# Optimization experiments

Measured on AMD Instinct MI355X. Metric: run time of the kernel, lower is better.

## Reference

```python
import jax, jax.numpy as jnp
import numpy as np

B, C, H, W = 256, 256, 16, 16   # batch, backbone channels, spatial (H*W = 256 = loop count)
E, NCLS = 128, 200              # opt.embed_size, opt.class_num

def _conv(x, w, stride, pad):
    # NCHW / OIHW conv, explicit torch-style symmetric padding
    return jax.lax.conv_general_dilated(x, w, (stride, stride), [(pad, pad), (pad, pad)],
                                        dimension_numbers=('NCHW', 'OIHW', 'NCHW'))

def _bn(x, s, b):
    # eval-mode BatchNorm folded to per-channel scale + shift
    return x * s[None, :, None, None] + b[None, :, None, None]

def setup_inputs() -> dict:
    key = jax.random.key(0)
    ks = jax.random.split(key, 12)
    f = lambda k, shape, scale: jax.random.normal(k, shape, jnp.float32) * scale
    bn_s = lambda k, n: 1.0 + 0.05 * jax.random.normal(k, (n,), jnp.float32)
    bn_b = lambda k, n: 0.05 * jax.random.normal(k, (n,), jnp.float32)
    return {
        'x': f(ks[0], (B, C, H, W), 1.0),
        'embed_w': f(ks[1], (E, C), 0.05),
        'embed_b': f(ks[2], (E,), 0.05),
        'b1_conv1': f(ks[3], (512, 256, 3, 3), 0.03),
        'b1_bn1_s': bn_s(jax.random.fold_in(key, 101), 512),
        'b1_bn1_b': bn_b(jax.random.fold_in(key, 102), 512),
        'b1_conv2': f(ks[4], (512, 512, 3, 3), 0.02),
        'b1_bn2_s': bn_s(jax.random.fold_in(key, 103), 512),
        'b1_bn2_b': bn_b(jax.random.fold_in(key, 104), 512),
        'b1_down_w': f(ks[5], (512, 256, 1, 1), 0.05),
        'b1_down_s': bn_s(jax.random.fold_in(key, 105), 512),
        'b1_down_b': bn_b(jax.random.fold_in(key, 106), 512),
        'b2_conv1': f(ks[6], (512, 512, 3, 3), 0.02),
        'b2_bn1_s': bn_s(jax.random.fold_in(key, 107), 512),
        'b2_bn1_b': bn_b(jax.random.fold_in(key, 108), 512),
        'b2_conv2': f(ks[7], (512, 512, 3, 3), 0.02),
        'b2_bn2_s': bn_s(jax.random.fold_in(key, 109), 512),
        'b2_bn2_b': bn_b(jax.random.fold_in(key, 110), 512),
        'head_w': f(ks[8], (NCLS, 512), 0.05),
    }

def reference(x, embed_w, embed_b,
              b1_conv1, b1_bn1_s, b1_bn1_b, b1_conv2, b1_bn2_s, b1_bn2_b,
              b1_down_w, b1_down_s, b1_down_b,
              b2_conv1, b2_bn1_s, b2_bn1_b, b2_conv2, b2_bn2_s, b2_bn2_b,
              head_w):
    # --- resblock = resnet layer4 (two BasicBlocks, 256->512, stride 2) ---
    y = jax.nn.relu(_bn(_conv(x, b1_conv1, 2, 1), b1_bn1_s, b1_bn1_b))
    y = _bn(_conv(y, b1_conv2, 1, 1), b1_bn2_s, b1_bn2_b)
    sc = _bn(_conv(x, b1_down_w, 2, 0), b1_down_s, b1_down_b)
    y = jax.nn.relu(y + sc)                              # [B,512,8,8]
    z = jax.nn.relu(_bn(_conv(y, b2_conv1, 1, 1), b2_bn1_s, b2_bn1_b))
    z = _bn(_conv(z, b2_conv2, 1, 1), b2_bn2_s, b2_bn2_b)
    z = jax.nn.relu(z + y)
    # --- class prediction: global avg pool + bias-free linear ---
    feat = jnp.mean(z, axis=(2, 3))                      # [B,512]
    prediction = feat @ head_w.T                         # [B,NCLS]
    # --- consistency: 1x1-conv embedding, then pairwise Gram + sigmoid ---
    emb = jnp.einsum('bchw,ec->behw', x, embed_w) + embed_b[None, :, None, None]
    emb = emb.reshape(B, E, H * W)                       # [B,E,256]
    inv_sqrt_e = jnp.float32(1.0 / np.sqrt(E))
    # vol[b,q,i] = sum_c emb[b,c,i]*emb[b,c,q] / sqrt(E)  (matches the 256-iter loop)
    vol = jax.nn.sigmoid(jnp.einsum('bei,beq->bqi', emb, emb) * inv_sqrt_e)
    return (prediction, vol)
```

## Files before the change

### kernel.cpp

```cpp
#include <hip/hip_runtime.h>


using short8 = __attribute__((ext_vector_type(8))) short;
using f32x4  = __attribute__((ext_vector_type(4))) float;
typedef unsigned short u16;
typedef unsigned int   u32;

#define MFMA(a,b,c) __builtin_amdgcn_mfma_f32_16x16x32_bf16((a),(b),(c),0,0,0)

__device__ __forceinline__ u16 f2b(float f){
    u32 u = __builtin_bit_cast(u32, f);
    u += 0x7FFFu + ((u >> 16) & 1u);
    return (u16)(u >> 16);
}
__device__ __forceinline__ float b2f(u16 h){
    u32 u = ((u32)h) << 16;
    return __builtin_bit_cast(float, u);
}
__device__ __forceinline__ u32 pack2(float a, float b){
    return (u32)f2b(a) | ((u32)f2b(b) << 16);
}
__device__ __forceinline__ float sigmoidf_(float v){
    return 1.0f / (1.0f + __expf(-v));
}

__global__ __launch_bounds__(256)
void prep_kernel(const float* __restrict__ w1, const float* __restrict__ s1,
                 const float* __restrict__ w2, const float* __restrict__ s2,
                 const float* __restrict__ w3, const float* __restrict__ s3,
                 const float* __restrict__ w4, const float* __restrict__ s4,
                 const float* __restrict__ wd, const float* __restrict__ sd,
                 const float* __restrict__ ew,
                 u16* __restrict__ wp1, u16* __restrict__ wp2,
                 u16* __restrict__ wp3, u16* __restrict__ wp4,
                 u16* __restrict__ wpd, u16* __restrict__ wpe)
{
    const int N2 = 9*16*512*40, N1 = 9*8*512*40, ND = 8*512*40, NE = 8*128*40;
    int t = blockIdx.x * 256 + threadIdx.x;
    if (t < N2) {
        int j = t % 40; int r = t / 40; int co = r & 511; int q = r >> 9;
        int cc = q & 15; int dydx = q >> 4;
        float v = (j < 32) ? w2[(co*512 + cc*32 + j)*9 + dydx] * s2[co] : 0.f;
        wp2[t] = f2b(v); return;
    }
    t -= N2;
    if (t < N2) {
        int j = t % 40; int r = t / 40; int co = r & 511; int q = r >> 9;
        int cc = q & 15; int dydx = q >> 4;
        float v = (j < 32) ? w3[(co*512 + cc*32 + j)*9 + dydx] * s3[co] : 0.f;
        wp3[t] = f2b(v); return;
    }
    t -= N2;
    if (t < N2) {
        int j = t % 40; int r = t / 40; int co = r & 511; int q = r >> 9;
        int cc = q & 15; int dydx = q >> 4;
        float v = (j < 32) ? w4[(co*512 + cc*32 + j)*9 + dydx] * s4[co] : 0.f;
        wp4[t] = f2b(v); return;
    }
    t -= N2;
    if (t < N1) {
        int j = t % 40; int r = t / 40; int co = r & 511; int q = r >> 9;
        int cc = q & 7; int dydx = q >> 3;
        float v = (j < 32) ? w1[(co*256 + cc*32 + j)*9 + dydx] * s1[co] : 0.f;
        wp1[t] = f2b(v); return;
    }
    t -= N1;
    if (t < ND) {
        int j = t % 40; int r = t / 40; int co = r & 511; int cc = r >> 9;
        float v = (j < 32) ? wd[co*256 + cc*32 + j] * sd[co] : 0.f;
        wpd[t] = f2b(v); return;
    }
    t -= ND;
    if (t < NE) {
        int j = t % 40; int r = t / 40; int e = r & 127; int cc = r >> 7;
        float v = (j < 32) ? ew[e*256 + cc*32 + j] : 0.f;
        wpe[t] = f2b(v);
    }
}

__global__ __launch_bounds__(512, 2)
void conv1_kernel(const float* __restrict__ x, const u16* __restrict__ wp,
                  const float* __restrict__ bnb, u16* __restrict__ out)
{
    const int cot = blockIdx.x;
    const int b0  = blockIdx.y * 2;
    const int tid = threadIdx.x;
    const int wid = tid >> 6, lane = tid & 63;
    const int ln = lane & 15, kg = lane >> 4;
    const int wco = wid >> 1;
    const int bb  = wid & 1;

    __shared__ u16 actb[2][2*289*40];

    {
        short8 zz = {0,0,0,0,0,0,0,0};
        short8* ab = (short8*)&actb[0][0];
        for (int j = tid; j < 2*2*289*40/8; j += 512) ab[j] = zz;
    }
    __syncthreads();

    auto stage_act = [&](int cc, int p){
        #pragma unroll
        for (int it = 0; it < 16; ++it){
            int f = it*512 + tid;
            int bb2 = f >> 12; int rem = f & 4095;
            int cip = rem >> 8; int px = rem & 255;
            const float* src = &x[(((size_t)(b0+bb2)*256 + cc*32 + 2*cip)*256) + px];
            float v0 = src[0], v1 = src[256];
            int r = ((px >> 4) + 1)*17 + (px & 15) + 1;
            *(u32*)&actb[p][(bb2*289 + r)*40 + 2*cip] = pack2(v0, v1);
        }
    };

    stage_act(0, 0);
    __syncthreads();

    f32x4 zero4 = {0.f,0.f,0.f,0.f};
    f32x4 acc[4][4];
    #pragma unroll
    for (int mf = 0; mf < 4; ++mf)
        #pragma unroll
        for (int nf = 0; nf < 4; ++nf) acc[mf][nf] = zero4;

    int bbase[4];
    #pragma unroll
    for (int nf = 0; nf < 4; ++nf){
        int px = nf*16 + ln;
        bbase[nf] = (bb*289 + 34*(px>>3) + 2*(px&7))*40 + kg*8;
    }

    for (int cc = 0; cc < 8; ++cc){
        if (cc < 7) stage_act(cc+1, (cc+1) & 1);
        const u16* abp = actb[cc & 1];
        #pragma unroll
        for (int d = 0; d < 9; ++d){
            const u16* wdp = wp + ((size_t)(d*8 + cc)*512 + cot*256)*40;
            int dy = d/3, dx = d - dy*3;
            int shift = (dy*17 + dx)*40;
            short8 A[4];
            #pragma unroll
            for (int mf = 0; mf < 4; ++mf)
                A[mf] = *(const short8*)&wdp[(wco*64 + mf*16 + ln)*40 + kg*8];
            #pragma unroll
            for (int nf = 0; nf < 4; ++nf){
                short8 B = *(const short8*)&abp[bbase[nf] + shift];
                #pragma unroll
                for (int mf = 0; mf < 4; ++mf)
                    acc[mf][nf] = MFMA(A[mf], B, acc[mf][nf]);
            }
        }
        __syncthreads();
    }

    #pragma unroll
    for (int mf = 0; mf < 4; ++mf){
        int co0 = cot*256 + wco*64 + mf*16 + kg*4;
        float4 bv = *(const float4*)&bnb[co0];
        #pragma unroll
        for (int nf = 0; nf < 4; ++nf){
            int px = nf*16 + ln;
            size_t o = (((size_t)(b0+bb)*64) + px)*512 + co0;
            f32x4 a = acc[mf][nf];
            ushort4 st;
            st.x = f2b(fmaxf(a[0] + bv.x, 0.f));
            st.y = f2b(fmaxf(a[1] + bv.y, 0.f));
            st.z = f2b(fmaxf(a[2] + bv.z, 0.f));
            st.w = f2b(fmaxf(a[3] + bv.w, 0.f));
            *(ushort4*)&out[o] = st;
        }
    }
}

template<int DOWN, int RES>
__global__ __launch_bounds__(64, 2)
void conv_s1_kernel(const u16* __restrict__ in, const u16* __restrict__ wp,
                    const float* __restrict__ bnb,
                    const float* __restrict__ x, const u16* __restrict__ wpd,
                    const float* __restrict__ dbb,
                    const u16* __restrict__ res, u16* __restrict__ out)
{
    const int b   = blockIdx.x;
    const int cot = blockIdx.y;
    const int lane = threadIdx.x;
    const int ln = lane & 15, kg = lane >> 4;

    __shared__ u16 actb[2][100*40];

    {
        short8 zz = {0,0,0,0,0,0,0,0};
        short8* ab = (short8*)&actb[0][0];
        #pragma unroll
        for (int it = 0; it < 16; ++it){
            int j = it*64 + lane;
            if (j < 1000) ab[j] = zz;
        }
    }

    int s_ld[4]; size_t s_go[4];
    #pragma unroll
    for (int it = 0; it < 4; ++it){
        int j = it*64 + lane;
        int px = j >> 2, cg = j & 3;
        s_ld[it] = (((px>>3)+1)*10 + (px&7) + 1)*40 + cg*8;
        s_go[it] = (((size_t)b*64 + px)*512) + cg*8;
    }

    short8 sreg[4];
    auto stage_load = [&](int cc){
        #pragma unroll
        for (int it = 0; it < 4; ++it)
            sreg[it] = *(const short8*)&in[s_go[it] + cc*32];
    };
    auto stage_store = [&](int p){
        #pragma unroll
        for (int it = 0; it < 4; ++it)
            *(short8*)&actb[p][s_ld[it]] = sreg[it];
    };

    stage_load(0); stage_store(0);

    f32x4 zero4 = {0.f,0.f,0.f,0.f};
    f32x4 acc[4][4];
    #pragma unroll
    for (int mf = 0; mf < 4; ++mf)
        #pragma unroll
        for (int nf = 0; nf < 4; ++nf) acc[mf][nf] = zero4;

    int bro[4];
    #pragma unroll
    for (int nf = 0; nf < 4; ++nf){
        int px = nf*16 + ln;
        bro[nf] = ((px>>3)*10 + (px&7))*40 + kg*8;
    }
    const int aoff = ln*40 + kg*8;
    const int abase = cot*64*40;

    for (int cc = 0; cc < 16; ++cc){
        if (cc < 15) stage_load(cc+1);
        const u16* abp = actb[cc & 1];
        #pragma unroll
        for (int dy = 0; dy < 3; ++dy){
            short8 A[3][4];
            #pragma unroll
            for (int dx = 0; dx < 3; ++dx){
                const u16* wdp = wp + (size_t)((dy*3+dx)*16 + cc)*512*40 + abase;
                #pragma unroll
                for (int mf = 0; mf < 4; ++mf)
                    A[dx][mf] = *(const short8*)&wdp[mf*640 + aoff];
            }
            #pragma unroll
            for (int dx = 0; dx < 3; ++dx){
                int shift = (dy*10 + dx)*40;
                #pragma unroll
                for (int nf = 0; nf < 4; ++nf){
                    short8 B = *(const short8*)&abp[bro[nf] + shift];
                    #pragma unroll
                    for (int mf = 0; mf < 4; ++mf)
                        acc[mf][nf] = MFMA(A[dx][mf], B, acc[mf][nf]);
                }
            }
        }
        if (cc < 15) stage_store((cc+1) & 1);
    }

    if (DOWN){
        for (int dc = 0; dc < 8; ++dc){
            #pragma unroll
            for (int it = 0; it < 16; ++it){
                int f = it*64 + lane;
                int cip = f >> 6, px2 = f & 63;
                int ipx = (px2>>3)*32 + (px2&7)*2;
                const float* src = &x[(((size_t)b*256 + dc*32 + 2*cip)*256) + ipx];
                *(u32*)&actb[0][px2*40 + cip*2] = pack2(src[0], src[256]);
            }
            const u16* wdp = wpd + (size_t)(dc*512)*40 + abase;
            short8 A[4];
            #pragma unroll
            for (int mf = 0; mf < 4; ++mf)
                A[mf] = *(const short8*)&wdp[mf*640 + aoff];
            #pragma unroll
            for (int nf = 0; nf < 4; ++nf){
                int rd = nf*16 + ln;
                short8 B = *(const short8*)&actb[0][rd*40 + kg*8];
                #pragma unroll
                for (int mf = 0; mf < 4; ++mf)
                    acc[mf][nf] = MFMA(A[mf], B, acc[mf][nf]);
            }
        }
    }

    #pragma unroll
    for (int mf = 0; mf < 4; ++mf){
        int co0 = cot*64 + mf*16 + kg*4;
        float4 bv = *(const float4*)&bnb[co0];
        if (DOWN){
            float4 dv = *(const float4*)&dbb[co0];
            bv.x += dv.x; bv.y += dv.y; bv.z += dv.z; bv.w += dv.w;
        }
        #pragma unroll
        for (int nf = 0; nf < 4; ++nf){
            int px = nf*16 + ln;
            size_t o = (((size_t)b*64) + px)*512 + co0;
            f32x4 a = acc[mf][nf];
            float v0 = a[0] + bv.x, v1 = a[1] + bv.y;
            float v2 = a[2] + bv.z, v3 = a[3] + bv.w;
            if (RES){
                ushort4 rv = *(const ushort4*)&res[o];
                v0 += b2f(rv.x); v1 += b2f(rv.y); v2 += b2f(rv.z); v3 += b2f(rv.w);
            }
            ushort4 st;
            st.x = f2b(fmaxf(v0, 0.f)); st.y = f2b(fmaxf(v1, 0.f));
            st.z = f2b(fmaxf(v2, 0.f)); st.w = f2b(fmaxf(v3, 0.f));
            *(ushort4*)&out[o] = st;
        }
    }
}

__global__ __launch_bounds__(256)
void head_kernel(const u16* __restrict__ z, const float* __restrict__ hw,
                 float* __restrict__ pred)
{
    const int b = blockIdx.x, tid = threadIdx.x;
    __shared__ float feat[512];
    float s0 = 0.f, s1 = 0.f;
    for (int px = 0; px < 64; ++px){
        u32 u = *(const u32*)&z[(((size_t)b*64 + px)*512) + 2*tid];
        s0 += b2f((u16)(u & 0xFFFF));
        s1 += b2f((u16)(u >> 16));
    }
    feat[2*tid]   = s0 * (1.f/64.f);
    feat[2*tid+1] = s1 * (1.f/64.f);
    __syncthreads();
    if (tid < 200){
        float acc = 0.f;
        const float4* hp = (const float4*)&hw[(size_t)tid*512];
        #pragma unroll 8
        for (int i = 0; i < 128; ++i){
            float4 h = hp[i];
            float4 f = *(const float4*)&feat[i*4];
            acc += h.x*f.x + h.y*f.y + h.z*f.z + h.w*f.w;
        }
        pred[b*200 + tid] = acc;
    }
}

__global__ __launch_bounds__(512, 2)
void gram_kernel(const float* __restrict__ x, const u16* __restrict__ wpe,
                 const float* __restrict__ eb, float* __restrict__ vol)
{
    const int b = blockIdx.x, tid = threadIdx.x;
    const int wid = tid >> 6, lane = tid & 63;
    const int ln = lane & 15, kg = lane >> 4;

    __shared__ u16 embl[256*136];
    __shared__ u16 xbl[256*40];
    __shared__ u16 ewl[128*40];

    f32x4 zero4 = {0.f,0.f,0.f,0.f};
    f32x4 ae[8][2];
    #pragma unroll
    for (int mf = 0; mf < 8; ++mf){ ae[mf][0] = zero4; ae[mf][1] = zero4; }

    for (int cc = 0; cc < 8; ++cc){
        __syncthreads();
        #pragma unroll
        for (int it = 0; it < 8; ++it){
            int f = it*512 + tid;
            int cip = f >> 8, px = f & 255;
            const float* src = &x[(((size_t)b*256 + cc*32 + 2*cip)*256) + px];
            *(u32*)&xbl[px*40 + 2*cip] = pack2(src[0], src[256]);
        }
        for (int j = tid; j < 640; j += 512)
            *(short8*)&ewl[j*8] = *(const short8*)&wpe[(cc*128)*40 + j*8];
        __syncthreads();
        short8 A[8];
        #pragma unroll
        for (int mf = 0; mf < 8; ++mf)
            A[mf] = *(const short8*)&ewl[(mf*16 + ln)*40 + kg*8];
        #pragma unroll
        for (int nf = 0; nf < 2; ++nf){
            short8 B = *(const short8*)&xbl[(wid*32 + nf*16 + ln)*40 + kg*8];
            #pragma unroll
            for (int mf = 0; mf < 8; ++mf)
                ae[mf][nf] = MFMA(A[mf], B, ae[mf][nf]);
        }
    }
    #pragma unroll
    for (int mf = 0; mf < 8; ++mf){
        int e0 = mf*16 + kg*4;
        float4 bv = *(const float4*)&eb[e0];
        #pragma unroll
        for (int nf = 0; nf < 2; ++nf){
            int px = wid*32 + nf*16 + ln;
            f32x4 a = ae[mf][nf];
            ushort4 st;
            st.x = f2b(a[0] + bv.x); st.y = f2b(a[1] + bv.y);
            st.z = f2b(a[2] + bv.z); st.w = f2b(a[3] + bv.w);
            *(ushort4*)&embl[px*136 + e0] = st;
        }
    }
    __syncthreads();

    const int wq = wid >> 2, wi = wid & 3;
    f32x4 g[8][4];
    #pragma unroll
    for (int mf = 0; mf < 8; ++mf)
        #pragma unroll
        for (int nf = 0; nf < 4; ++nf) g[mf][nf] = zero4;

    #pragma unroll
    for (int ks = 0; ks < 4; ++ks){
        short8 A[8];
        #pragma unroll
        for (int mf = 0; mf < 8; ++mf)
            A[mf] = *(const short8*)&embl[(wq*128 + mf*16 + ln)*136 + ks*32 + kg*8];
        #pragma unroll
        for (int nf = 0; nf < 4; ++nf){
            short8 B = *(const short8*)&embl[(wi*64 + nf*16 + ln)*136 + ks*32 + kg*8];
            #pragma unroll
            for (int mf = 0; mf < 8; ++mf)
                g[mf][nf] = MFMA(A[mf], B, g[mf][nf]);
        }
    }
    const float sc = 0.08838834764831845f;
    #pragma unroll
    for (int mf = 0; mf < 8; ++mf){
        #pragma unroll
        for (int nf = 0; nf < 4; ++nf){
            int i = wi*64 + nf*16 + ln;
            #pragma unroll
            for (int r = 0; r < 4; ++r){
                int q = wq*128 + mf*16 + kg*4 + r;
                vol[(((size_t)b*256 + q)*256) + i] = sigmoidf_(g[mf][nf][r] * sc);
            }
        }
    }
}

extern "C" void kernel_launch(void* const* d_in, const int* in_sizes, int n_in,
                              void* d_out, int out_size, void* d_ws, size_t ws_size,
                              hipStream_t stream)
{
    const float* x    = (const float*)d_in[0];
    const float* ew   = (const float*)d_in[1];
    const float* eb   = (const float*)d_in[2];
    const float* w1   = (const float*)d_in[3];
    const float* bn1s = (const float*)d_in[4];
    const float* bn1b = (const float*)d_in[5];
    const float* w2   = (const float*)d_in[6];
    const float* bn2s = (const float*)d_in[7];
    const float* bn2b = (const float*)d_in[8];
    const float* wd   = (const float*)d_in[9];
    const float* bnds = (const float*)d_in[10];
    const float* bndb = (const float*)d_in[11];
    const float* w3   = (const float*)d_in[12];
    const float* bn3s = (const float*)d_in[13];
    const float* bn3b = (const float*)d_in[14];
    const float* w4   = (const float*)d_in[15];
    const float* bn4s = (const float*)d_in[16];
    const float* bn4b = (const float*)d_in[17];
    const float* hw   = (const float*)d_in[18];

    float* pred = (float*)d_out;
    float* vol  = pred + 51200;

    u16* wp2 = (u16*)d_ws;
    u16* wp3 = wp2 + 2949120;
    u16* wp4 = wp3 + 2949120;
    u16* wp1 = wp4 + 2949120;
    u16* wpd = wp1 + 1474560;
    u16* wpe = wpd + 163840;

    u16* y1 = (u16*)vol;
    u16* y  = y1 + 8388608;
    u16* z1 = y  + 8388608;
    u16* z  = z1 + 8388608;

    prep_kernel<<<41120, 256, 0, stream>>>(w1, bn1s, w2, bn2s, w3, bn3s, w4, bn4s,
                                           wd, bnds, ew, wp1, wp2, wp3, wp4, wpd, wpe);
    conv1_kernel<<<dim3(2,128), 512, 0, stream>>>(x, wp1, bn1b, y1);
    conv_s1_kernel<1,0><<<dim3(256,8), 64, 0, stream>>>(y1, wp2, bn2b, x, wpd, bndb,
                                                        nullptr, y);
    conv_s1_kernel<0,0><<<dim3(256,8), 64, 0, stream>>>(y, wp3, bn3b, nullptr, nullptr,
                                                        nullptr, nullptr, z1);
    conv_s1_kernel<0,1><<<dim3(256,8), 64, 0, stream>>>(z1, wp4, bn4b, nullptr, nullptr,
                                                        nullptr, y, z);
    head_kernel<<<256, 256, 0, stream>>>(z, hw, pred);
    gram_kernel<<<256, 512, 0, stream>>>(x, wpe, eb, vol);
}
```

Measured before the change: 400.4 us.

## Software-pipeline conv weight loads across taps and pad LDS rows

The stride-1 conv kernel now issues each 3x3 tap's weight-fragment loads one tap ahead, rotating through three register buffers, so global loads overlap the MFMAs of the current tap. The LDS activation row stride grows from 40 to 42 elements to reduce bank conflicts on B-fragment reads. MFMA blocks are wrapped in s_setprio to favour the math wave. The risks are misaligned 128-bit LDS accesses at the 84-byte row stride, harmless out-of-range prefetches on the final channel chunk, and more register pressure.

```diff
diff --git a/kernel.cpp b/kernel.cpp
--- a/kernel.cpp
+++ b/kernel.cpp
@@ -171,6 +171,21 @@
     }
 }
 
+#define CONV_STEP(Acur, Aload, ccl, dl, dy_, dx_)                       \
+    loadA(Aload, (ccl), (dl));                                          \
+    __builtin_amdgcn_s_setprio(1);                                      \
+    {                                                                   \
+        const int shift_ = ((dy_)*10 + (dx_))*42;                       \
+        _Pragma("unroll")                                               \
+        for (int nf = 0; nf < 4; ++nf){                                 \
+            short8 Bv = *(const short8*)&abp[bro[nf] + shift_];         \
+            _Pragma("unroll")                                           \
+            for (int mf = 0; mf < 4; ++mf)                              \
+                acc[mf][nf] = MFMA(Acur[mf], Bv, acc[mf][nf]);          \
+        }                                                               \
+    }                                                                   \
+    __builtin_amdgcn_s_setprio(0);
+
 template<int DOWN, int RES>
 __global__ __launch_bounds__(64, 2)
 void conv_s1_kernel(const u16* __restrict__ in, const u16* __restrict__ wp,
@@ -184,15 +199,15 @@
     const int lane = threadIdx.x;
     const int ln = lane & 15, kg = lane >> 4;
 
-    __shared__ u16 actb[2][100*40];
+    __shared__ u16 actb[2][100*42];
 
     {
         short8 zz = {0,0,0,0,0,0,0,0};
         short8* ab = (short8*)&actb[0][0];
         #pragma unroll
-        for (int it = 0; it < 16; ++it){
+        for (int it = 0; it < 17; ++it){
             int j = it*64 + lane;
-            if (j < 1000) ab[j] = zz;
+            if (j < 1050) ab[j] = zz;
         }
     }
 
@@ -201,7 +216,7 @@
     for (int it = 0; it < 4; ++it){
         int j = it*64 + lane;
         int px = j >> 2, cg = j & 3;
-        s_ld[it] = (((px>>3)+1)*10 + (px&7) + 1)*40 + cg*8;
+        s_ld[it] = (((px>>3)+1)*10 + (px&7) + 1)*42 + cg*8;
         s_go[it] = (((size_t)b*64 + px)*512) + cg*8;
     }
 
@@ -217,7 +232,20 @@
             *(short8*)&actb[p][s_ld[it]] = sreg[it];
     };
 
+    const int aoff = ln*40 + kg*8;
+    const int abase = cot*64*40;
+    auto loadA = [&](short8* A, int cc, int d){
+        const u16* wdp = wp + (size_t)(d*16 + cc)*512*40 + abase;
+        #pragma unroll
+        for (int mf = 0; mf < 4; ++mf)
+            A[mf] = *(const short8*)&wdp[mf*640 + aoff];
+    };
+
     stage_load(0); stage_store(0);
+
+    short8 A0[4], A1[4], A2[4];
+    loadA(A0, 0, 0);
+    loadA(A1, 0, 1);
 
     f32x4 zero4 = {0.f,0.f,0.f,0.f};
     f32x4 acc[4][4];
@@ -230,36 +258,21 @@
     #pragma unroll
     for (int nf = 0; nf < 4; ++nf){
         int px = nf*16 + ln;
-        bro[nf] = ((px>>3)*10 + (px&7))*40 + kg*8;
-    }
-    const int aoff = ln*40 + kg*8;
-    const int abase = cot*64*40;
+        bro[nf] = ((px>>3)*10 + (px&7))*42 + kg*8;
+    }
 
     for (int cc = 0; cc < 16; ++cc){
         if (cc < 15) stage_load(cc+1);
         const u16* abp = actb[cc & 1];
-        #pragma unroll
-        for (int dy = 0; dy < 3; ++dy){
-            short8 A[3][4];
-            #pragma unroll
-            for (int dx = 0; dx < 3; ++dx){
-                const u16* wdp = wp + (size_t)((dy*3+dx)*16 + cc)*512*40 + abase;
-                #pragma unroll
-                for (int mf = 0; mf < 4; ++mf)
-                    A[dx][mf] = *(const short8*)&wdp[mf*640 + aoff];
-            }
-            #pragma unroll
-            for (int dx = 0; dx < 3; ++dx){
-                int shift = (dy*10 + dx)*40;
-                #pragma unroll
-                for (int nf = 0; nf < 4; ++nf){
-                    short8 B = *(const short8*)&abp[bro[nf] + shift];
-                    #pragma unroll
-                    for (int mf = 0; mf < 4; ++mf)
-                        acc[mf][nf] = MFMA(A[dx][mf], B, acc[mf][nf]);
-                }
-            }
-        }
+        CONV_STEP(A0, A2, cc,   2, 0,0)
+        CONV_STEP(A1, A0, cc,   3, 0,1)
+        CONV_STEP(A2, A1, cc,   4, 0,2)
+        CONV_STEP(A0, A2, cc,   5, 1,0)
+        CONV_STEP(A1, A0, cc,   6, 1,1)
+        CONV_STEP(A2, A1, cc,   7, 1,2)
+        CONV_STEP(A0, A2, cc,   8, 2,0)
+        CONV_STEP(A1, A0, cc+1, 0, 2,1)
+        CONV_STEP(A2, A1, cc+1, 1, 2,2)
         if (cc < 15) stage_store((cc+1) & 1);
     }
 
@@ -271,21 +284,23 @@
                 int cip = f >> 6, px2 = f & 63;
                 int ipx = (px2>>3)*32 + (px2&7)*2;
                 const float* src = &x[(((size_t)b*256 + dc*32 + 2*cip)*256) + ipx];
-                *(u32*)&actb[0][px2*40 + cip*2] = pack2(src[0], src[256]);
+                *(u32*)&actb[0][px2*42 + cip*2] = pack2(src[0], src[256]);
             }
             const u16* wdp = wpd + (size_t)(dc*512)*40 + abase;
             short8 A[4];
             #pragma unroll
             for (int mf = 0; mf < 4; ++mf)
                 A[mf] = *(const short8*)&wdp[mf*640 + aoff];
+            __builtin_amdgcn_s_setprio(1);
             #pragma unroll
             for (int nf = 0; nf < 4; ++nf){
                 int rd = nf*16 + ln;
-                short8 B = *(const short8*)&actb[0][rd*40 + kg*8];
+                short8 B = *(const short8*)&actb[0][rd*42 + kg*8];
                 #pragma unroll
                 for (int mf = 0; mf < 4; ++mf)
                     acc[mf][nf] = MFMA(A[mf], B, acc[mf][nf]);
             }
+            __builtin_amdgcn_s_setprio(0);
         }
     }
 
```

Result: slower. 574.1 us (+43.4%).

## Split stride-1 conv blocks spatially in half and raise occupancy

Applied to the files above, without the earlier changes.

Each conv_s1 block now computes 32 output pixels (half the 8x8 image) instead of 64. The grid doubles to 4096 one-wave blocks, and the block index is remapped so neighbouring blocks share a batch image. Halving the accumulators, dropping the double-buffered LDS tile for a single 6-row halo tile, and raising launch_bounds to 4 waves per SIMD are meant to increase occupancy and latency hiding. The cost is that each weight fragment now feeds half as many MFMAs, so weight loads per unit of work double, and staging loads are no longer overlapped through a second buffer.

```diff
diff --git a/kernel.cpp b/kernel.cpp
--- a/kernel.cpp
+++ b/kernel.cpp
@@ -172,63 +172,68 @@
 }
 
 template<int DOWN, int RES>
-__global__ __launch_bounds__(64, 2)
+__global__ __launch_bounds__(64, 4)
 void conv_s1_kernel(const u16* __restrict__ in, const u16* __restrict__ wp,
                     const float* __restrict__ bnb,
                     const float* __restrict__ x, const u16* __restrict__ wpd,
                     const float* __restrict__ dbb,
                     const u16* __restrict__ res, u16* __restrict__ out)
 {
-    const int b   = blockIdx.x;
-    const int cot = blockIdx.y;
+    const int bid  = blockIdx.x;
+    const int half = (bid >> 3) & 1;
+    const int cot  = (bid >> 4) & 7;
+    const int b    = (bid & 7) | ((bid >> 7) << 3);
     const int lane = threadIdx.x;
     const int ln = lane & 15, kg = lane >> 4;
 
-    __shared__ u16 actb[2][100*40];
+    __shared__ u16 actb[60*40];
 
     {
         short8 zz = {0,0,0,0,0,0,0,0};
-        short8* ab = (short8*)&actb[0][0];
-        #pragma unroll
-        for (int it = 0; it < 16; ++it){
+        short8* ab = (short8*)&actb[0];
+        #pragma unroll
+        for (int it = 0; it < 5; ++it){
             int j = it*64 + lane;
-            if (j < 1000) ab[j] = zz;
-        }
-    }
-
-    int s_ld[4]; size_t s_go[4];
-    #pragma unroll
-    for (int it = 0; it < 4; ++it){
+            if (j < 300) ab[j] = zz;
+        }
+    }
+
+    int s_ld[3]; size_t s_go[3]; bool s_on[3];
+    #pragma unroll
+    for (int it = 0; it < 3; ++it){
         int j = it*64 + lane;
-        int px = j >> 2, cg = j & 3;
-        s_ld[it] = (((px>>3)+1)*10 + (px&7) + 1)*40 + cg*8;
-        s_go[it] = (((size_t)b*64 + px)*512) + cg*8;
-    }
-
-    short8 sreg[4];
+        s_on[it] = (j < 160);
+        int jj = s_on[it] ? j : 0;
+        int pxl = jj >> 2, cg = jj & 3;
+        int iy = pxl >> 3, ix = pxl & 7;
+        int iy_img = iy + half*3;
+        int lrow = iy*10 + ix + 1 + (1-half)*10;
+        s_ld[it] = lrow*40 + cg*8;
+        s_go[it] = (((size_t)b*64 + iy_img*8 + ix)*512) + cg*8;
+    }
+
+    short8 sreg[3];
     auto stage_load = [&](int cc){
         #pragma unroll
-        for (int it = 0; it < 4; ++it)
-            sreg[it] = *(const short8*)&in[s_go[it] + cc*32];
+        for (int it = 0; it < 3; ++it)
+            if (s_on[it]) sreg[it] = *(const short8*)&in[s_go[it] + cc*32];
     };
-    auto stage_store = [&](int p){
-        #pragma unroll
-        for (int it = 0; it < 4; ++it)
-            *(short8*)&actb[p][s_ld[it]] = sreg[it];
+    auto stage_store = [&](){
+        #pragma unroll
+        for (int it = 0; it < 3; ++it)
+            if (s_on[it]) *(short8*)&actb[s_ld[it]] = sreg[it];
     };
 
-    stage_load(0); stage_store(0);
+    stage_load(0); stage_store();
 
     f32x4 zero4 = {0.f,0.f,0.f,0.f};
-    f32x4 acc[4][4];
-    #pragma unroll
-    for (int mf = 0; mf < 4; ++mf)
-        #pragma unroll
-        for (int nf = 0; nf < 4; ++nf) acc[mf][nf] = zero4;
-
-    int bro[4];
-    #pragma unroll
-    for (int nf = 0; nf < 4; ++nf){
+    f32x4 acc[4][2];
+    #pragma unroll
+    for (int mf = 0; mf < 4; ++mf){ acc[mf][0] = zero4; acc[mf][1] = zero4; }
+
+    int bro[2];
+    #pragma unroll
+    for (int nf = 0; nf < 2; ++nf){
         int px = nf*16 + ln;
         bro[nf] = ((px>>3)*10 + (px&7))*40 + kg*8;
     }
@@ -237,7 +242,6 @@
 
     for (int cc = 0; cc < 16; ++cc){
         if (cc < 15) stage_load(cc+1);
-        const u16* abp = actb[cc & 1];
         #pragma unroll
         for (int dy = 0; dy < 3; ++dy){
             short8 A[3][4];
@@ -252,26 +256,27 @@
             for (int dx = 0; dx < 3; ++dx){
                 int shift = (dy*10 + dx)*40;
                 #pragma unroll
-                for (int nf = 0; nf < 4; ++nf){
-                    short8 B = *(const short8*)&abp[bro[nf] + shift];
+                for (int nf = 0; nf < 2; ++nf){
+                    short8 B = *(const short8*)&actb[bro[nf] + shift];
                     #pragma unroll
                     for (int mf = 0; mf < 4; ++mf)
                         acc[mf][nf] = MFMA(A[dx][mf], B, acc[mf][nf]);
                 }
             }
         }
-        if (cc < 15) stage_store((cc+1) & 1);
+        if (cc < 15) stage_store();
     }
 
     if (DOWN){
         for (int dc = 0; dc < 8; ++dc){
             #pragma unroll
-            for (int it = 0; it < 16; ++it){
+            for (int it = 0; it < 8; ++it){
                 int f = it*64 + lane;
-                int cip = f >> 6, px2 = f & 63;
-                int ipx = (px2>>3)*32 + (px2&7)*2;
+                int cip = f >> 5, px2 = f & 31;
+                int pxg = half*32 + px2;
+                int ipx = (pxg>>3)*32 + (pxg&7)*2;
                 const float* src = &x[(((size_t)b*256 + dc*32 + 2*cip)*256) + ipx];
-                *(u32*)&actb[0][px2*40 + cip*2] = pack2(src[0], src[256]);
+                *(u32*)&actb[px2*40 + cip*2] = pack2(src[0], src[256]);
             }
             const u16* wdp = wpd + (size_t)(dc*512)*40 + abase;
             short8 A[4];
@@ -279,9 +284,9 @@
             for (int mf = 0; mf < 4; ++mf)
                 A[mf] = *(const short8*)&wdp[mf*640 + aoff];
             #pragma unroll
-            for (int nf = 0; nf < 4; ++nf){
+            for (int nf = 0; nf < 2; ++nf){
                 int rd = nf*16 + ln;
-                short8 B = *(const short8*)&actb[0][rd*40 + kg*8];
+                short8 B = *(const short8*)&actb[rd*40 + kg*8];
                 #pragma unroll
                 for (int mf = 0; mf < 4; ++mf)
                     acc[mf][nf] = MFMA(A[mf], B, acc[mf][nf]);
@@ -298,9 +303,9 @@
             bv.x += dv.x; bv.y += dv.y; bv.z += dv.z; bv.w += dv.w;
         }
         #pragma unroll
-        for (int nf = 0; nf < 4; ++nf){
-            int px = nf*16 + ln;
-            size_t o = (((size_t)b*64) + px)*512 + co0;
+        for (int nf = 0; nf < 2; ++nf){
+            int pxg = half*32 + nf*16 + ln;
+            size_t o = (((size_t)b*64) + pxg)*512 + co0;
             f32x4 a = acc[mf][nf];
             float v0 = a[0] + bv.x, v1 = a[1] + bv.y;
             float v2 = a[2] + bv.z, v3 = a[3] + bv.w;
@@ -479,12 +484,12 @@
     prep_kernel<<<41120, 256, 0, stream>>>(w1, bn1s, w2, bn2s, w3, bn3s, w4, bn4s,
                                            wd, bnds, ew, wp1, wp2, wp3, wp4, wpd, wpe);
     conv1_kernel<<<dim3(2,128), 512, 0, stream>>>(x, wp1, bn1b, y1);
-    conv_s1_kernel<1,0><<<dim3(256,8), 64, 0, stream>>>(y1, wp2, bn2b, x, wpd, bndb,
-                                                        nullptr, y);
-    conv_s1_kernel<0,0><<<dim3(256,8), 64, 0, stream>>>(y, wp3, bn3b, nullptr, nullptr,
-                                                        nullptr, nullptr, z1);
-    conv_s1_kernel<0,1><<<dim3(256,8), 64, 0, stream>>>(z1, wp4, bn4b, nullptr, nullptr,
-                                                        nullptr, y, z);
+    conv_s1_kernel<1,0><<<4096, 64, 0, stream>>>(y1, wp2, bn2b, x, wpd, bndb,
+                                                 nullptr, y);
+    conv_s1_kernel<0,0><<<4096, 64, 0, stream>>>(y, wp3, bn3b, nullptr, nullptr,
+                                                 nullptr, nullptr, z1);
+    conv_s1_kernel<0,1><<<4096, 64, 0, stream>>>(z1, wp4, bn4b, nullptr, nullptr,
+                                                 nullptr, y, z);
     head_kernel<<<256, 256, 0, stream>>>(z, hw, pred);
     gram_kernel<<<256, 512, 0, stream>>>(x, wpe, eb, vol);
 }
```

Result: slower. 443.7 us (+10.8%).
